# Optimization experiments

Measured on AMD Instinct MI355X. Metric: run time of the kernel, lower is better.

The kernel has to match this reference:

```python
import jax, jax.numpy as jnp
import numpy as np

B, N, K_OUT, NBASIS, NGLOBALS, H = 16, 2048, 128, 4, 2, 256
DIN = 1 + NBASIS + N + NGLOBALS  # norm + basis projections + all-pairs dots + globals
NEG_SLOPE = 0.01  # torch LeakyReLU default


def setup_inputs() -> dict:
    key = jax.random.key(0)
    ks = jax.random.split(key, 6)
    x = jax.random.uniform(ks[0], (B, N, 3), jnp.float32)      # positions -> dots >= 0
    u = jax.random.normal(ks[1], (B, NGLOBALS), jnp.float32)
    basis = jax.random.normal(ks[2], (B, NBASIS, 3), jnp.float32)
    def init_w(k, fan_in, fan_out):
        return jax.random.normal(k, (fan_in, fan_out), jnp.float32) / np.float32(np.sqrt(fan_in))
    W1 = init_w(ks[3], DIN, H); b1 = jnp.zeros((H,), jnp.float32)
    W2 = init_w(ks[4], H, H);   b2 = jnp.zeros((H,), jnp.float32)
    W3 = init_w(ks[5], H, K_OUT); b3 = jnp.zeros((K_OUT,), jnp.float32)
    return {"x": x, "u": u, "basis": basis,
            "W1": W1, "b1": b1, "W2": W2, "b2": b2, "W3": W3, "b3": b3}


def reference(x, u, basis, W1, b1, W2, b2, W3, b3):
    # per-vector norms: [B, N, 1]
    norms = jnp.linalg.norm(x, axis=-1, keepdims=True)
    # projections onto basis vectors: [B, N, NBASIS]
    proj = jnp.einsum('bid,bnd->bin', x, basis)
    # all-pairs sqrt of dot products: [B, N, N]
    dots = jnp.sqrt(jnp.einsum('bid,bjd->bij', x, x))
    # concat order matches original: globals first, then [norm, proj, dots]
    u_rep = jnp.broadcast_to(u[:, None, :], (B, N, NGLOBALS))
    scalars = jnp.concatenate([u_rep, norms, proj, dots], axis=-1)  # [B, N, DIN]
    # MLP (Linear -> LeakyReLU -> Linear -> LeakyReLU -> Linear)
    h = jax.nn.leaky_relu(scalars @ W1 + b1, NEG_SLOPE)
    h = jax.nn.leaky_relu(h @ W2 + b2, NEG_SLOPE)
    fk = h @ W3 + b3  # [B, N, K_OUT]
    # outer product with x followed by mean over input vecs, fused into one einsum
    # (avoids materializing the [B, N, K_OUT, 3] tensor)
    return jnp.einsum('bio,bid->bod', fk, x) / np.float32(N)  # [B, K_OUT, 3]
```

## Files before the change

kernel.cpp:

```cpp
#include <hip/hip_runtime.h>

typedef unsigned short u16;
typedef unsigned int   u32;

typedef __attribute__((ext_vector_type(8))) short short8;
typedef __attribute__((ext_vector_type(4))) float floatx4;
typedef __attribute__((ext_vector_type(2))) float v2f;

__device__ __forceinline__ u16 f2bf(float f) {
    u32 u = __float_as_uint(f);
    u = u + 0x7fffu + ((u >> 16) & 1u);
    return (u16)(u >> 16);
}

__device__ __forceinline__ u32 pack2bf(float s0, float s1) {
    u32 a = __float_as_uint(s0) + 0x8000u;
    u32 b = __float_as_uint(s1) + 0x8000u;
    return __builtin_amdgcn_perm(b, a, 0x07060302u);
}

__device__ __forceinline__ floatx4 mfma16(short8 a, short8 b, floatx4 c) {
    return __builtin_amdgcn_mfma_f32_16x16x32_bf16(a, b, c, 0, 0, 0);
}

__global__ void k_prep(const float* __restrict__ W1, const float* __restrict__ W2,
                       const float* __restrict__ W3, u16* __restrict__ W1frag,
                       u16* __restrict__ W2frag, u16* __restrict__ W3frag) {
    int idx = blockIdx.x * 256 + threadIdx.x;
    if (idx < 524288) {
        int kt = idx >> 13, r = idx & 8191;
        int t = r >> 4, j = (r >> 3) & 1, ji = r & 7;
        int lane = t & 63, w = t >> 6, lr = lane & 15, lq = lane >> 4;
        W1frag[idx] = f2bf(W1[(7 + kt * 32 + lq * 8 + ji) * 256 + w * 32 + j * 16 + lr]);
    } else if (idx < 589824) {
        int i = idx - 524288;
        int kt = i >> 13, r = i & 8191;
        int t = r >> 5, jj = (r >> 3) & 3, ji = r & 7;
        int lane = t & 63, wv = t >> 6, lr = lane & 15, lq = lane >> 4;
        W2frag[i] = f2bf(W2[(kt * 32 + lq * 8 + ji) * 256 + wv * 64 + jj * 16 + lr]);
    } else if (idx < 622592) {
        int i = idx - 589824;
        int kt = i >> 12, r = i & 4095;
        int t = r >> 4, j = (r >> 3) & 1, ji = r & 7;
        int lane = t & 63, wv = t >> 6, lr = lane & 15, lq = lane >> 4;
        W3frag[i] = f2bf(W3[(kt * 32 + lq * 8 + ji) * 128 + wv * 32 + j * 16 + lr]);
    }
}

__global__ __launch_bounds__(512, 4) void k_h1(
    const float* __restrict__ x, const float* __restrict__ u,
    const float* __restrict__ basis, const float* __restrict__ W1,
    const float* __restrict__ b1, const u16* __restrict__ W1frag,
    u16* __restrict__ h1) {
    __shared__ float xls[6144];
    __shared__ u16 As[2][64][32];
    __shared__ float rowsml[64][6];
    __shared__ float colsml[256][6];

    const int t = threadIdx.x;
    const int b = blockIdx.y;
    const int i0 = blockIdx.x * 64;
    const int lane = t & 63, w = t >> 6;
    const int lr = lane & 15, lq = lane >> 4;

    {
        const float4* src = (const float4*)(x + b * 6144);
#pragma unroll
        for (int kk = 0; kk < 3; ++kk) {
            int q = t + kk * 512;
            float4 v = src[q];
            float vv[4] = {v.x, v.y, v.z, v.w};
            int e = q * 4;
#pragma unroll
            for (int cc = 0; cc < 4; ++cc) {
                int ee = e + cc;
                xls[(ee % 3) * 2048 + ee / 3] = vv[cc];
            }
        }
    }
    if (t < 256) {
        int c = t;
        float u0 = u[b * 2 + 0], u1 = u[b * 2 + 1];
        colsml[c][0] = b1[c] + u0 * W1[c] + u1 * W1[256 + c];
        colsml[c][1] = W1[512 + c];
        colsml[c][2] = W1[768 + c];
        colsml[c][3] = W1[1024 + c];
        colsml[c][4] = W1[1280 + c];
        colsml[c][5] = W1[1536 + c];
    }
    __syncthreads();
    if (t < 64) {
        float xx = xls[i0 + t], xy = xls[2048 + i0 + t], xz = xls[4096 + i0 + t];
        rowsml[t][0] = sqrtf(xx * xx + xy * xy + xz * xz);
#pragma unroll
        for (int p = 0; p < 4; ++p) {
            const float* bp = basis + (b * 4 + p) * 3;
            rowsml[t][1 + p] = xx * bp[0] + xy * bp[1] + xz * bp[2];
        }
    }
    const float ax = xls[i0 + lane];
    const float ay = xls[2048 + i0 + lane];
    const float az = xls[4096 + i0 + lane];
    const u16* wf = W1frag + t * 16;
    const float4* X4 = (const float4*)xls;

    char* Asb = (char*)As;
    char* aswp = Asb + lane * 64 + ((w ^ (lane >> 3)) << 3);
    int roff[4];
#pragma unroll
    for (int i = 0; i < 4; ++i)
        roff[i] = (i * 16 + lr) * 64 + (((lq << 1) ^ (2 * i + (lr >> 3))) << 3);

    auto gen_store = [&](int kt, int buf) {
        int q = kt * 8 + w;
        float4 xv = X4[q], yv = X4[512 + q], zv = X4[1024 + q];
        v2f xlo = {xv.x, xv.y}, xhi = {xv.z, xv.w};
        v2f ylo = {yv.x, yv.y}, yhi = {yv.z, yv.w};
        v2f zlo = {zv.x, zv.y}, zhi = {zv.z, zv.w};
        v2f dlo = xlo * ax, dhi = xhi * ax;
        dlo += ylo * ay; dhi += yhi * ay;
        dlo += zlo * az; dhi += zhi * az;
        float s0 = __builtin_amdgcn_sqrtf(dlo.x);
        float s1 = __builtin_amdgcn_sqrtf(dlo.y);
        float s2 = __builtin_amdgcn_sqrtf(dhi.x);
        float s3 = __builtin_amdgcn_sqrtf(dhi.y);
        uint2 dv; dv.x = pack2bf(s0, s1); dv.y = pack2bf(s2, s3);
        *(uint2*)(aswp + buf * 4096) = dv;
    };

    auto load_frags = [&](int buf, short8* dst) {
#pragma unroll
        for (int i = 0; i < 4; ++i) {
            union { short8 s; uint2 u2[2]; } f;
            f.u2[0] = *(const uint2*)(Asb + buf * 4096 + roff[i]);
            f.u2[1] = *(const uint2*)(Asb + buf * 4096 + (roff[i] ^ 8));
            dst[i] = f.s;
        }
    };

    floatx4 acc[4][2];
    const floatx4 zero = {0.f, 0.f, 0.f, 0.f};
#pragma unroll
    for (int i = 0; i < 4; ++i)
#pragma unroll
        for (int j = 0; j < 2; ++j) acc[i][j] = zero;

    short8 acur[4], bcur[2], bnxt[2];
    gen_store(0, 0);
#pragma unroll
    for (int j = 0; j < 2; ++j) bcur[j] = *(const short8*)(wf + j * 8);
    __syncthreads();
    load_frags(0, acur);

#pragma unroll 2
    for (int kt = 0; kt < 64; ++kt) {
        if (kt < 63) {
            const u16* wn = wf + (kt + 1) * 8192;
#pragma unroll
            for (int j = 0; j < 2; ++j) bnxt[j] = *(const short8*)(wn + j * 8);
            gen_store(kt + 1, (kt + 1) & 1);
        }
#pragma unroll
        for (int i = 0; i < 4; ++i)
#pragma unroll
            for (int j = 0; j < 2; ++j)
                acc[i][j] = mfma16(acur[i], bcur[j], acc[i][j]);
        __syncthreads();
        if (kt < 63) {
            load_frags((kt + 1) & 1, acur);
#pragma unroll
            for (int j = 0; j < 2; ++j) bcur[j] = bnxt[j];
        }
    }

    const int c0 = w * 32 + lr, c1 = c0 + 16;
    float c0v[6], c1v[6];
#pragma unroll
    for (int q = 0; q < 6; ++q) { c0v[q] = colsml[c0][q]; c1v[q] = colsml[c1][q]; }
#pragma unroll
    for (int i = 0; i < 4; ++i) {
#pragma unroll
        for (int r = 0; r < 4; ++r) {
            int row = i * 16 + lq * 4 + r;
            float nrm = rowsml[row][0];
            float p0 = rowsml[row][1], p1 = rowsml[row][2];
            float p2 = rowsml[row][3], p3 = rowsml[row][4];
            u16* orow = h1 + (b * 2048 + i0 + row) * 256;
            float v0 = acc[i][0][r] + c0v[0] + nrm * c0v[1] +
                       p0 * c0v[2] + p1 * c0v[3] + p2 * c0v[4] + p3 * c0v[5];
            v0 = v0 > 0.f ? v0 : 0.01f * v0;
            orow[c0] = f2bf(v0);
            float v1 = acc[i][1][r] + c1v[0] + nrm * c1v[1] +
                       p0 * c1v[2] + p1 * c1v[3] + p2 * c1v[4] + p3 * c1v[5];
            v1 = v1 > 0.f ? v1 : 0.01f * v1;
            orow[c1] = f2bf(v1);
        }
    }
}

__global__ __launch_bounds__(256, 2) void k_tail(
    const u16* __restrict__ h1, const u16* __restrict__ W2frag,
    const float* __restrict__ b2, const u16* __restrict__ W3frag,
    const float* __restrict__ b3, const float* __restrict__ x,
    float* __restrict__ out) {
    __shared__ u16 h2s[64][264];
    __shared__ float colb2[256];
    __shared__ float colb3[128];
    __shared__ float xs[64][4];
    __shared__ float red[128][4];

    const int t = threadIdx.x;
    const int m0 = blockIdx.x * 64;
    const int b = m0 >> 11, i0 = m0 & 2047;
    const int lane = t & 63, wv = t >> 6;
    const int lr = lane & 15, lq = lane >> 4;

    colb2[t] = b2[t];
    if (t < 128) colb3[t] = b3[t];
    if (t < 64) {
        const float* xp = x + (b * 2048 + i0 + t) * 3;
        xs[t][0] = xp[0]; xs[t][1] = xp[1]; xs[t][2] = xp[2];
    }

    floatx4 acc[4][4];
    const floatx4 zero = {0.f, 0.f, 0.f, 0.f};
#pragma unroll
    for (int i = 0; i < 4; ++i)
#pragma unroll
        for (int j = 0; j < 4; ++j) acc[i][j] = zero;

    const u16* hsrc = h1 + m0 * 256 + lr * 256 + lq * 8;
    const u16* w2s = W2frag + t * 32;
#pragma unroll 2
    for (int kt = 0; kt < 8; ++kt) {
        short8 af[4], bf[4];
#pragma unroll
        for (int i = 0; i < 4; ++i)
            af[i] = *(const short8*)(hsrc + i * 4096 + kt * 32);
#pragma unroll
        for (int j = 0; j < 4; ++j)
            bf[j] = *(const short8*)(w2s + kt * 8192 + j * 8);
#pragma unroll
        for (int i = 0; i < 4; ++i)
#pragma unroll
            for (int j = 0; j < 4; ++j) acc[i][j] = mfma16(af[i], bf[j], acc[i][j]);
    }
#pragma unroll
    for (int i = 0; i < 4; ++i)
#pragma unroll
        for (int r = 0; r < 4; ++r) {
            int row = i * 16 + lq * 4 + r;
#pragma unroll
            for (int j = 0; j < 4; ++j) {
                int col = wv * 64 + j * 16 + lr;
                float v = acc[i][j][r] + colb2[col];
                v = v > 0.f ? v : 0.01f * v;
                h2s[row][col] = f2bf(v);
            }
        }
    __syncthreads();

    floatx4 acc2[4][2];
#pragma unroll
    for (int i = 0; i < 4; ++i)
#pragma unroll
        for (int j = 0; j < 2; ++j) acc2[i][j] = zero;

    const u16* w3s = W3frag + t * 16;
#pragma unroll 2
    for (int kt = 0; kt < 8; ++kt) {
        short8 af[4], bf[2];
#pragma unroll
        for (int i = 0; i < 4; ++i)
            af[i] = *(const short8*)&h2s[i * 16 + lr][kt * 32 + lq * 8];
#pragma unroll
        for (int j = 0; j < 2; ++j)
            bf[j] = *(const short8*)(w3s + kt * 4096 + j * 8);
#pragma unroll
        for (int i = 0; i < 4; ++i)
#pragma unroll
            for (int j = 0; j < 2; ++j) acc2[i][j] = mfma16(af[i], bf[j], acc2[i][j]);
    }

    float s[2][3];
#pragma unroll
    for (int j = 0; j < 2; ++j) { s[j][0] = 0.f; s[j][1] = 0.f; s[j][2] = 0.f; }
#pragma unroll
    for (int i = 0; i < 4; ++i)
#pragma unroll
        for (int r = 0; r < 4; ++r) {
            int row = i * 16 + lq * 4 + r;
            float x0 = xs[row][0], x1 = xs[row][1], x2 = xs[row][2];
#pragma unroll
            for (int j = 0; j < 2; ++j) {
                int col = wv * 32 + j * 16 + lr;
                float fk = acc2[i][j][r] + colb3[col];
                s[j][0] += fk * x0; s[j][1] += fk * x1; s[j][2] += fk * x2;
            }
        }
#pragma unroll
    for (int j = 0; j < 2; ++j)
#pragma unroll
        for (int d = 0; d < 3; ++d) {
            float v = s[j][d];
            v += __shfl_xor(v, 16);
            v += __shfl_xor(v, 32);
            if (lane < 16) red[wv * 32 + j * 16 + lane][d] = v;
        }
    __syncthreads();
    if (t < 128) {
#pragma unroll
        for (int d = 0; d < 3; ++d)
            atomicAdd(&out[(b * 128 + t) * 3 + d], red[t][d] * (1.0f / 2048.0f));
    }
}

extern "C" void kernel_launch(void* const* d_in, const int* in_sizes, int n_in,
                              void* d_out, int out_size, void* d_ws, size_t ws_size,
                              hipStream_t stream) {
    const float* x     = (const float*)d_in[0];
    const float* u     = (const float*)d_in[1];
    const float* basis = (const float*)d_in[2];
    const float* W1    = (const float*)d_in[3];
    const float* b1    = (const float*)d_in[4];
    const float* W2    = (const float*)d_in[5];
    const float* b2    = (const float*)d_in[6];
    const float* W3    = (const float*)d_in[7];
    const float* b3    = (const float*)d_in[8];
    float* out = (float*)d_out;

    char* ws = (char*)d_ws;
    u16*  W1frag = (u16*)ws;
    u16*  W2frag = (u16*)(ws + 1048576);
    u16*  W3frag = (u16*)(ws + 1179648);
    u16*  h1     = (u16*)(ws + 1245184);

    hipMemsetAsync(out, 0, 24576, stream);
    k_prep<<<2432, 256, 0, stream>>>(W1, W2, W3, W1frag, W2frag, W3frag);
    k_h1<<<dim3(32, 16), 512, 0, stream>>>(x, u, basis, W1, b1, W1frag, h1);
    k_tail<<<512, 256, 0, stream>>>(h1, W2frag, b2, W3frag, b3, x, out);
}
```

Before: 142.0 us.

## Double K-step per iteration in h1 GEMM with wider LDS tiles

```diff
diff --git a/kernel.cpp b/kernel.cpp
--- a/kernel.cpp
+++ b/kernel.cpp
@@ -53,7 +53,7 @@
     const float* __restrict__ b1, const u16* __restrict__ W1frag,
     u16* __restrict__ h1) {
     __shared__ float xls[6144];
-    __shared__ u16 As[2][64][32];
+    __shared__ u16 As[2][64][64];
     __shared__ float rowsml[64][6];
     __shared__ float colsml[256][6];
 
@@ -105,36 +105,48 @@
     const float4* X4 = (const float4*)xls;
 
     char* Asb = (char*)As;
-    char* aswp = Asb + lane * 64 + ((w ^ (lane >> 3)) << 3);
-    int roff[4];
-#pragma unroll
-    for (int i = 0; i < 4; ++i)
-        roff[i] = (i * 16 + lr) * 64 + (((lq << 1) ^ (2 * i + (lr >> 3))) << 3);
-
-    auto gen_store = [&](int kt, int buf) {
-        int q = kt * 8 + w;
-        float4 xv = X4[q], yv = X4[512 + q], zv = X4[1024 + q];
-        v2f xlo = {xv.x, xv.y}, xhi = {xv.z, xv.w};
-        v2f ylo = {yv.x, yv.y}, yhi = {yv.z, yv.w};
-        v2f zlo = {zv.x, zv.y}, zhi = {zv.z, zv.w};
-        v2f dlo = xlo * ax, dhi = xhi * ax;
-        dlo += ylo * ay; dhi += yhi * ay;
-        dlo += zlo * az; dhi += zhi * az;
-        float s0 = __builtin_amdgcn_sqrtf(dlo.x);
-        float s1 = __builtin_amdgcn_sqrtf(dlo.y);
-        float s2 = __builtin_amdgcn_sqrtf(dhi.x);
-        float s3 = __builtin_amdgcn_sqrtf(dhi.y);
-        uint2 dv; dv.x = pack2bf(s0, s1); dv.y = pack2bf(s2, s3);
-        *(uint2*)(aswp + buf * 4096) = dv;
+    char* aswp = Asb + lane * 128 + ((w ^ (lane & 7)) << 4);
+    int ro[4];
+    {
+        int s0 = (lq ^ (lr & 7));
+#pragma unroll
+        for (int i = 0; i < 4; ++i)
+            ro[i] = (i * 16 + lr) * 128 + (s0 << 4);
+    }
+
+    auto gen_store = [&](int s, int buf) {
+        int q = s * 16 + w * 2;
+        float4 xv0 = X4[q],        xv1 = X4[q + 1];
+        float4 yv0 = X4[512 + q],  yv1 = X4[513 + q];
+        float4 zv0 = X4[1024 + q], zv1 = X4[1025 + q];
+        v2f xA = {xv0.x, xv0.y}, xB = {xv0.z, xv0.w};
+        v2f xC = {xv1.x, xv1.y}, xD = {xv1.z, xv1.w};
+        v2f yA = {yv0.x, yv0.y}, yB = {yv0.z, yv0.w};
+        v2f yC = {yv1.x, yv1.y}, yD = {yv1.z, yv1.w};
+        v2f zA = {zv0.x, zv0.y}, zB = {zv0.z, zv0.w};
+        v2f zC = {zv1.x, zv1.y}, zD = {zv1.z, zv1.w};
+        v2f dA = xA * ax, dB = xB * ax, dC = xC * ax, dD = xD * ax;
+        dA += yA * ay; dB += yB * ay; dC += yC * ay; dD += yD * ay;
+        dA += zA * az; dB += zB * az; dC += zC * az; dD += zD * az;
+        float s0 = __builtin_amdgcn_sqrtf(dA.x);
+        float s1 = __builtin_amdgcn_sqrtf(dA.y);
+        float s2 = __builtin_amdgcn_sqrtf(dB.x);
+        float s3 = __builtin_amdgcn_sqrtf(dB.y);
+        float s4 = __builtin_amdgcn_sqrtf(dC.x);
+        float s5 = __builtin_amdgcn_sqrtf(dC.y);
+        float s6 = __builtin_amdgcn_sqrtf(dD.x);
+        float s7 = __builtin_amdgcn_sqrtf(dD.y);
+        uint4 dv;
+        dv.x = pack2bf(s0, s1); dv.y = pack2bf(s2, s3);
+        dv.z = pack2bf(s4, s5); dv.w = pack2bf(s6, s7);
+        *(uint4*)(aswp + buf * 8192) = dv;
     };
 
     auto load_frags = [&](int buf, short8* dst) {
 #pragma unroll
         for (int i = 0; i < 4; ++i) {
-            union { short8 s; uint2 u2[2]; } f;
-            f.u2[0] = *(const uint2*)(Asb + buf * 4096 + roff[i]);
-            f.u2[1] = *(const uint2*)(Asb + buf * 4096 + (roff[i] ^ 8));
-            dst[i] = f.s;
+            dst[i]     = *(const short8*)(Asb + buf * 8192 + ro[i]);
+            dst[4 + i] = *(const short8*)(Asb + buf * 8192 + (ro[i] ^ 64));
         }
     };
 
@@ -145,31 +157,39 @@
 #pragma unroll
         for (int j = 0; j < 2; ++j) acc[i][j] = zero;
 
-    short8 acur[4], bcur[2], bnxt[2];
+    short8 acur[8], bcur[4], bnxt[4];
     gen_store(0, 0);
 #pragma unroll
-    for (int j = 0; j < 2; ++j) bcur[j] = *(const short8*)(wf + j * 8);
+    for (int kk = 0; kk < 2; ++kk)
+#pragma unroll
+        for (int j = 0; j < 2; ++j)
+            bcur[kk * 2 + j] = *(const short8*)(wf + kk * 8192 + j * 8);
     __syncthreads();
     load_frags(0, acur);
 
 #pragma unroll 2
-    for (int kt = 0; kt < 64; ++kt) {
-        if (kt < 63) {
-            const u16* wn = wf + (kt + 1) * 8192;
-#pragma unroll
-            for (int j = 0; j < 2; ++j) bnxt[j] = *(const short8*)(wn + j * 8);
-            gen_store(kt + 1, (kt + 1) & 1);
-        }
-#pragma unroll
-        for (int i = 0; i < 4; ++i)
-#pragma unroll
-            for (int j = 0; j < 2; ++j)
-                acc[i][j] = mfma16(acur[i], bcur[j], acc[i][j]);
+    for (int s = 0; s < 32; ++s) {
+        if (s < 31) {
+            const u16* wn = wf + (2 * (s + 1)) * 8192;
+#pragma unroll
+            for (int kk = 0; kk < 2; ++kk)
+#pragma unroll
+                for (int j = 0; j < 2; ++j)
+                    bnxt[kk * 2 + j] = *(const short8*)(wn + kk * 8192 + j * 8);
+            gen_store(s + 1, (s + 1) & 1);
+        }
+#pragma unroll
+        for (int kk = 0; kk < 2; ++kk)
+#pragma unroll
+            for (int i = 0; i < 4; ++i)
+#pragma unroll
+                for (int j = 0; j < 2; ++j)
+                    acc[i][j] = mfma16(acur[kk * 4 + i], bcur[kk * 2 + j], acc[i][j]);
         __syncthreads();
-        if (kt < 63) {
-            load_frags((kt + 1) & 1, acur);
-#pragma unroll
-            for (int j = 0; j < 2; ++j) bcur[j] = bnxt[j];
+        if (s < 31) {
+            load_frags((s + 1) & 1, acur);
+#pragma unroll
+            for (int j = 0; j < 4; ++j) bcur[j] = bnxt[j];
         }
     }
 
```

After: 172.1 us. 1.21x slower.
